# Performance work log

Hardware: AMD Instinct MI355X
Metric: run time of the kernel (lower is better)

Reference implementation:

```python
import jax, jax.numpy as jnp
import numpy as np

B, T = 32, 50
H, D, V = 1024, 512, 50257


def setup_inputs() -> dict:
    key = jax.random.key(0)
    ks = jax.random.split(key, 8)
    s = 0.05  # small init scale to keep LSTM gates in a sane range
    return {
        "inputs": jax.random.normal(ks[0], (B, H), jnp.float32),          # initial hidden state
        "targets": jax.random.randint(ks[1], (B, T), 0, V, jnp.int32),     # teacher-forcing tokens
        "emb": jax.random.normal(ks[2], (V, D), jnp.float32) * s,
        "W_ih": jax.random.normal(ks[3], (4 * H, D), jnp.float32) * s,     # torch gate order i,f,g,o
        "W_hh": jax.random.normal(ks[4], (4 * H, H), jnp.float32) * s,
        "b_ih": jnp.zeros((4 * H,), jnp.float32),
        "b_hh": jnp.zeros((4 * H,), jnp.float32),
        "W_proj": jax.random.normal(ks[5], (V, H), jnp.float32) * s,
        "b_proj": jnp.zeros((V,), jnp.float32),
    }


def reference(inputs, targets, emb, W_ih, W_hh, b_ih, b_hh, W_proj, b_proj):
    b, t = targets.shape
    h = inputs.shape[1]
    # decoder input tokens: BOS(=1) at step 0, then targets shifted right by one
    tok = jnp.concatenate([jnp.ones((b, 1), targets.dtype), targets[:, :-1]], axis=1)  # [B,T]
    x = emb[tok]  # [B,T,D]
    # precompute input contribution to all gates for every step
    xg = jnp.einsum("btd,gd->btg", x, W_ih) + b_ih + b_hh  # [B,T,4H]

    def step(carry, xg_t):
        hs, cs = carry
        g = xg_t + hs @ W_hh.T  # [B,4H]
        i = jax.nn.sigmoid(g[:, :h])
        f = jax.nn.sigmoid(g[:, h:2 * h])
        gg = jnp.tanh(g[:, 2 * h:3 * h])
        o = jax.nn.sigmoid(g[:, 3 * h:])
        cs = f * cs + i * gg
        hs = o * jnp.tanh(cs)
        return (hs, cs), hs

    c0 = jnp.zeros_like(inputs)
    _, hs = jax.lax.scan(step, (inputs, c0), jnp.swapaxes(xg, 0, 1))  # hs: [T,B,H]
    hs = jnp.swapaxes(hs, 0, 1)  # [B,T,H]
    logits = jnp.einsum("bth,vh->btv", hs, W_proj) + b_proj  # [B,T,V]
    predictions = jnp.argmax(logits, axis=-1)  # [B,T]
    return logits, predictions
```

## Files before the change

kernel.cpp:

```cpp
#include <hip/hip_runtime.h>
#include <math.h>

#define BB 32
#define TT 50
#define HH 1024
#define DD 512
#define VV 50257
#define G4H 4096

typedef __attribute__((ext_vector_type(8))) short bf16x8;
typedef __attribute__((ext_vector_type(8))) unsigned short u16x8;
typedef __attribute__((ext_vector_type(4))) float f32x4;

__device__ inline unsigned short f2bf(float x) {
    unsigned u = __float_as_uint(x);
    u = (u + 0x7fff + ((u >> 16) & 1)) >> 16;
    return (unsigned short)u;
}
__device__ inline float bf2f(unsigned short h) {
    return __uint_as_float(((unsigned)h) << 16);
}
__device__ inline void gl16(const void* g, void* l) {
    __builtin_amdgcn_global_load_lds(
        (const __attribute__((address_space(1))) unsigned int*)g,
        (__attribute__((address_space(3))) unsigned int*)l, 16, 0, 0);
}

__global__ void split_f32(const float* __restrict__ x,
                          unsigned short* __restrict__ hi,
                          unsigned short* __restrict__ lo, long n4) {
    long i = (long)blockIdx.x * 256 + threadIdx.x;
    long stride = (long)gridDim.x * 256;
    for (; i < n4; i += stride) {
        float4 v = ((const float4*)x)[i];
        ushort4 h, l;
        h.x = f2bf(v.x); l.x = f2bf(v.x - bf2f(h.x));
        h.y = f2bf(v.y); l.y = f2bf(v.y - bf2f(h.y));
        h.z = f2bf(v.z); l.z = f2bf(v.z - bf2f(h.z));
        h.w = f2bf(v.w); l.w = f2bf(v.w - bf2f(h.w));
        ((ushort4*)hi)[i] = h;
        ((ushort4*)lo)[i] = l;
    }
}

__global__ void xg_gemm(const int* __restrict__ targets,
                        const float* __restrict__ emb,
                        const float* __restrict__ W_ih,
                        const float* __restrict__ b_ih,
                        const float* __restrict__ b_hh,
                        float* __restrict__ xg) {
    __shared__ float As[16][65];
    __shared__ float Bs[16][65];
    const int m0 = blockIdx.y * 64;
    const int n0 = blockIdx.x * 64;
    const int tid = threadIdx.x;
    const int tx = tid & 15;
    const int ty = tid >> 4;
    const int lk = tx;
    const int lm = ty;

    const float* arow[4];
    const float* brow[4];
#pragma unroll
    for (int i = 0; i < 4; i++) {
        int bt = m0 + lm + i * 16;
        int b = bt / TT, t = bt % TT;
        int tok = (t == 0) ? 1 : targets[b * TT + (t - 1)];
        arow[i] = emb + (size_t)tok * DD;
        int n = n0 + lm + i * 16;
        brow[i] = W_ih + (size_t)n * DD;
    }

    float acc[4][4] = {};
    for (int k0 = 0; k0 < DD; k0 += 16) {
#pragma unroll
        for (int i = 0; i < 4; i++) As[lk][lm + i * 16] = arow[i][k0 + lk];
#pragma unroll
        for (int i = 0; i < 4; i++) Bs[lk][lm + i * 16] = brow[i][k0 + lk];
        __syncthreads();
#pragma unroll
        for (int k = 0; k < 16; k++) {
            float a[4], bb[4];
#pragma unroll
            for (int i = 0; i < 4; i++) a[i] = As[k][ty + i * 16];
#pragma unroll
            for (int j = 0; j < 4; j++) bb[j] = Bs[k][tx + j * 16];
#pragma unroll
            for (int i = 0; i < 4; i++)
#pragma unroll
                for (int j = 0; j < 4; j++) acc[i][j] += a[i] * bb[j];
        }
        __syncthreads();
    }
#pragma unroll
    for (int i = 0; i < 4; i++) {
        int m = m0 + ty + i * 16;
#pragma unroll
        for (int j = 0; j < 4; j++) {
            int n = n0 + tx + j * 16;
            xg[(size_t)m * G4H + n] = acc[i][j] + b_ih[n] + b_hh[n];
        }
    }
}

#define NH 16
__global__ __launch_bounds__(512, 2) void lstm_mfma(
    const unsigned short* __restrict__ Wh, const unsigned short* __restrict__ Wl,
    const float* __restrict__ xg,
    const unsigned short* __restrict__ hin_h, const unsigned short* __restrict__ hin_l,
    long hin_stride,
    float* __restrict__ c_buf,
    unsigned short* __restrict__ Ah, unsigned short* __restrict__ Al,
    int t) {
    __shared__ unsigned short sW[2][2][2][64 * 64];
    __shared__ unsigned short sH[2][2][2][32 * 64];
    __shared__ float gbuf[8][32][17];
    const int tid = threadIdx.x;
    const int w = tid >> 6;
    const int g = w & 3;
    const int h2 = w >> 2;
    const int l = tid & 63;
    const int lr = l & 15, lk = l >> 4;
    const int nh0 = blockIdx.x * NH;

    const int stid = tid & 255;
    const int sh2 = tid >> 8;
    const int kbase = sh2 * 512;

    const int wrow = stid >> 2;
    const int ws0 = (stid & 3) * 2;
    const int wg = wrow >> 4, wj = wrow & 15;
    const unsigned short* gWh = Wh + (size_t)(wg * HH + nh0 + wj) * HH + kbase + ws0 * 8;
    const unsigned short* gWl = Wl + (size_t)(wg * HH + nh0 + wj) * HH + kbase + ws0 * 8;
    const int wwb0 = wrow * 64 + ((ws0) ^ (wrow & 7)) * 8;
    const int wwb1 = wrow * 64 + ((ws0 + 1) ^ (wrow & 7)) * 8;

    const int hp = stid & 127;
    const int hrow = hp >> 2;
    const int hs0 = (hp & 3) * 2;
    const unsigned short* gH =
        ((stid < 128) ? hin_h : hin_l) + (size_t)hrow * hin_stride + kbase + hs0 * 8;
    const int hsel = (stid < 128) ? 0 : 1;
    const int hwb0 = hrow * 64 + ((hs0) ^ (hrow & 7)) * 8;
    const int hwb1 = hrow * 64 + ((hs0 + 1) ^ (hrow & 7)) * 8;

    f32x4 acc0 = (f32x4){0.f, 0.f, 0.f, 0.f};
    f32x4 acc1 = (f32x4){0.f, 0.f, 0.f, 0.f};

    u16x8 rWh0 = *(const u16x8*)gWh, rWh1 = *(const u16x8*)(gWh + 8);
    u16x8 rWl0 = *(const u16x8*)gWl, rWl1 = *(const u16x8*)(gWl + 8);
    u16x8 rH0  = *(const u16x8*)gH,  rH1  = *(const u16x8*)(gH + 8);
    *(u16x8*)&sW[sh2][0][0][wwb0] = rWh0; *(u16x8*)&sW[sh2][0][0][wwb1] = rWh1;
    *(u16x8*)&sW[sh2][0][1][wwb0] = rWl0; *(u16x8*)&sW[sh2][0][1][wwb1] = rWl1;
    if (hsel == 0) { *(u16x8*)&sH[sh2][0][0][hwb0] = rH0; *(u16x8*)&sH[sh2][0][0][hwb1] = rH1; }
    else           { *(u16x8*)&sH[sh2][0][1][hwb0] = rH0; *(u16x8*)&sH[sh2][0][1][hwb1] = rH1; }
    rWh0 = *(const u16x8*)(gWh + 64); rWh1 = *(const u16x8*)(gWh + 64 + 8);
    rWl0 = *(const u16x8*)(gWl + 64); rWl1 = *(const u16x8*)(gWl + 64 + 8);
    rH0  = *(const u16x8*)(gH + 64);  rH1  = *(const u16x8*)(gH + 64 + 8);

    int cur = 0;
#pragma unroll 1
    for (int it = 0; it < 8; it++) {
        __syncthreads();
        if (it < 7) {
            const int nxt = cur ^ 1;
            *(u16x8*)&sW[sh2][nxt][0][wwb0] = rWh0; *(u16x8*)&sW[sh2][nxt][0][wwb1] = rWh1;
            *(u16x8*)&sW[sh2][nxt][1][wwb0] = rWl0; *(u16x8*)&sW[sh2][nxt][1][wwb1] = rWl1;
            if (hsel == 0) { *(u16x8*)&sH[sh2][nxt][0][hwb0] = rH0; *(u16x8*)&sH[sh2][nxt][0][hwb1] = rH1; }
            else           { *(u16x8*)&sH[sh2][nxt][1][hwb0] = rH0; *(u16x8*)&sH[sh2][nxt][1][hwb1] = rH1; }
            const int kn = (it < 6) ? (it + 2) * 64 : 0;
            rWh0 = *(const u16x8*)(gWh + kn); rWh1 = *(const u16x8*)(gWh + kn + 8);
            rWl0 = *(const u16x8*)(gWl + kn); rWl1 = *(const u16x8*)(gWl + kn + 8);
            rH0  = *(const u16x8*)(gH + kn);  rH1  = *(const u16x8*)(gH + kn + 8);
        }
#pragma unroll
        for (int kk = 0; kk < 2; kk++) {
            const int rsl = ((kk * 4 + lk) ^ (lr & 7)) * 8;
            bf16x8 bh = *(const bf16x8*)&sW[h2][cur][0][(g * 16 + lr) * 64 + rsl];
            bf16x8 bl = *(const bf16x8*)&sW[h2][cur][1][(g * 16 + lr) * 64 + rsl];
            bf16x8 a0h = *(const bf16x8*)&sH[h2][cur][0][lr * 64 + rsl];
            bf16x8 a1h = *(const bf16x8*)&sH[h2][cur][0][(16 + lr) * 64 + rsl];
            bf16x8 a0l = *(const bf16x8*)&sH[h2][cur][1][lr * 64 + rsl];
            bf16x8 a1l = *(const bf16x8*)&sH[h2][cur][1][(16 + lr) * 64 + rsl];
            acc0 = __builtin_amdgcn_mfma_f32_16x16x32_bf16(a0h, bh, acc0, 0, 0, 0);
            acc0 = __builtin_amdgcn_mfma_f32_16x16x32_bf16(a0h, bl, acc0, 0, 0, 0);
            acc0 = __builtin_amdgcn_mfma_f32_16x16x32_bf16(a0l, bh, acc0, 0, 0, 0);
            acc1 = __builtin_amdgcn_mfma_f32_16x16x32_bf16(a1h, bh, acc1, 0, 0, 0);
            acc1 = __builtin_amdgcn_mfma_f32_16x16x32_bf16(a1h, bl, acc1, 0, 0, 0);
            acc1 = __builtin_amdgcn_mfma_f32_16x16x32_bf16(a1l, bh, acc1, 0, 0, 0);
        }
        cur ^= 1;
    }

    __syncthreads();
#pragma unroll
    for (int r = 0; r < 4; r++) {
        gbuf[w][lk * 4 + r][lr] = acc0[r];
        gbuf[w][16 + lk * 4 + r][lr] = acc1[r];
    }
    __syncthreads();

    {
        int b = tid >> 4, j = tid & 15;
        size_t xb = ((size_t)b * TT + t) * G4H + nh0 + j;
        float gi_ = gbuf[0][b][j] + gbuf[4][b][j] + xg[xb];
        float gf_ = gbuf[1][b][j] + gbuf[5][b][j] + xg[xb + HH];
        float gg_ = gbuf[2][b][j] + gbuf[6][b][j] + xg[xb + 2 * HH];
        float go_ = gbuf[3][b][j] + gbuf[7][b][j] + xg[xb + 3 * HH];

        float i_ = 1.f / (1.f + expf(-gi_));
        float f_ = 1.f / (1.f + expf(-gf_));
        float g_ = tanhf(gg_);
        float o_ = 1.f / (1.f + expf(-go_));

        int ci = b * HH + nh0 + j;
        float c_old = (t == 0) ? 0.f : c_buf[ci];
        float c_new = f_ * c_old + i_ * g_;
        float h_new = o_ * tanhf(c_new);
        c_buf[ci] = c_new;

        size_t ho = ((size_t)b * TT + t) * HH + nh0 + j;
        unsigned short hh = f2bf(h_new);
        Ah[ho] = hh;
        Al[ho] = f2bf(h_new - bf2f(hh));
    }
}

__global__ void lstm_step(const float* __restrict__ W_hh,
                          const float* __restrict__ xg,
                          const float* __restrict__ h_prev,
                          float* __restrict__ c_buf,
                          float* __restrict__ h_out,
                          float* __restrict__ hs_all,
                          int t) {
    __shared__ float h_s[32][68];
    __shared__ float w_s[32][68];
    const int tid = threadIdx.x;
    const int b = tid & 31;
    const int jl = tid >> 5;
    const int n0 = blockIdx.x * 8;
    const int n = n0 + jl;

    float acc[4] = {0.f, 0.f, 0.f, 0.f};
    for (int k0 = 0; k0 < HH; k0 += 64) {
#pragma unroll
        for (int i = 0; i < 2; i++) {
            int e = tid + i * 256;
            int r = e >> 4;
            int c = e & 15;
            float4 hv = *(const float4*)&h_prev[r * HH + k0 + c * 4];
            *(float4*)&h_s[r][c * 4] = hv;
            int gi = r >> 3, jj = r & 7;
            float4 wv = *(const float4*)&W_hh[(size_t)(gi * HH + n0 + jj) * HH + k0 + c * 4];
            *(float4*)&w_s[r][c * 4] = wv;
        }
        __syncthreads();
#pragma unroll
        for (int k = 0; k < 64; k += 4) {
            float4 hv = *(const float4*)&h_s[b][k];
            float4 w0 = *(const float4*)&w_s[jl][k];
            float4 w1 = *(const float4*)&w_s[8 + jl][k];
            float4 w2 = *(const float4*)&w_s[16 + jl][k];
            float4 w3 = *(const float4*)&w_s[24 + jl][k];
            acc[0] += hv.x * w0.x + hv.y * w0.y + hv.z * w0.z + hv.w * w0.w;
            acc[1] += hv.x * w1.x + hv.y * w1.y + hv.z * w1.z + hv.w * w1.w;
            acc[2] += hv.x * w2.x + hv.y * w2.y + hv.z * w2.z + hv.w * w2.w;
            acc[3] += hv.x * w3.x + hv.y * w3.y + hv.z * w3.z + hv.w * w3.w;
        }
        __syncthreads();
    }

    const int bt = b * TT + t;
    float gi_ = acc[0] + xg[(size_t)bt * G4H + n];
    float gf_ = acc[1] + xg[(size_t)bt * G4H + HH + n];
    float gg_ = acc[2] + xg[(size_t)bt * G4H + 2 * HH + n];
    float go_ = acc[3] + xg[(size_t)bt * G4H + 3 * HH + n];

    float i_ = 1.f / (1.f + expf(-gi_));
    float f_ = 1.f / (1.f + expf(-gf_));
    float g_ = tanhf(gg_);
    float o_ = 1.f / (1.f + expf(-go_));

    float c_old = (t == 0) ? 0.f : c_buf[b * HH + n];
    float c_new = f_ * c_old + i_ * g_;
    float h_new = o_ * tanhf(c_new);

    c_buf[b * HH + n] = c_new;
    h_out[b * HH + n] = h_new;
    hs_all[(size_t)bt * HH + n] = h_new;
}

__global__ __launch_bounds__(256, 4) void proj_mfma(
    const unsigned short* __restrict__ Ah, const unsigned short* __restrict__ Al,
    const unsigned short* __restrict__ Bh, const unsigned short* __restrict__ Bl,
    const float* __restrict__ b_proj, float* __restrict__ logits) {
    __shared__ __attribute__((aligned(16))) unsigned short sA[2][128 * 32];
    __shared__ __attribute__((aligned(16))) unsigned short sB[2][128 * 32];
    const int tid = threadIdx.x;
    const int w = tid >> 6;
    const int l = tid & 63;
    const int wr = w >> 1, wc = w & 1;
    const int lr = l & 15, lk = l >> 4;

    const int d = blockIdx.x;
    const int xcd = d & 7;
    const int k = d >> 3;
    const int ncnt = (xcd == 0) ? 50 : 49;
    const int nstart = (xcd == 0) ? 0 : 50 + (xcd - 1) * 49;
    if (k >= 13 * ncnt) return;
    const int per4 = 4 * ncnt;
    int s, rr_;
    if (k < per4)          { s = 0; rr_ = k; }
    else if (k < 2 * per4) { s = 1; rr_ = k - per4; }
    else if (k < 3 * per4) { s = 2; rr_ = k - 2 * per4; }
    else                   { s = 3; rr_ = k - 3 * per4; }
    const int ssize = (s == 3) ? 1 : 4;
    const int nloc = rr_ / ssize;
    const int mins = rr_ - nloc * ssize;
    const int m0 = (s * 4 + mins) * 128;
    const int n0 = (nstart + nloc) * 128;

    const unsigned short* garr = (w == 0) ? Ah : (w == 1) ? Al : (w == 2) ? Bh : Bl;
    unsigned short* larr = (w == 0) ? sA[0] : (w == 1) ? sA[1]
                         : (w == 2) ? sB[0] : sB[1];
    const int isA = (w < 2);
    const unsigned short* gsrc[8];
#pragma unroll
    for (int i = 0; i < 8; i++) {
        int r = i * 16 + (l >> 2);
        int sl = (l & 3) ^ ((r >> 1) & 3);
        int g = isA ? (m0 + r) : (n0 + r);
        int gmax = isA ? (BB * TT - 1) : (VV - 1);
        if (g > gmax) g = gmax;
        gsrc[i] = garr + (size_t)g * HH + sl * 8;
    }

    const int rswz = (lk ^ ((lr >> 1) & 3)) * 8;

    f32x4 acc[4][4];
#pragma unroll
    for (int i = 0; i < 4; i++)
#pragma unroll
        for (int j = 0; j < 4; j++) acc[i][j] = (f32x4){0.f, 0.f, 0.f, 0.f};

#pragma unroll 1
    for (int it = 0; it < 32; it++) {
        const int k0v = it * 32;
#pragma unroll
        for (int i = 0; i < 8; i++)
            gl16(gsrc[i] + k0v, larr + i * 512);
        __syncthreads();

        bf16x8 ah[4], al[4], bh[4], bl[4];
#pragma unroll
        for (int i = 0; i < 4; i++) {
            int ra = (wr * 64 + i * 16 + lr) * 32 + rswz;
            ah[i] = *(const bf16x8*)&sA[0][ra];
            al[i] = *(const bf16x8*)&sA[1][ra];
        }
#pragma unroll
        for (int j = 0; j < 4; j++) {
            int rb = (wc * 64 + j * 16 + lr) * 32 + rswz;
            bh[j] = *(const bf16x8*)&sB[0][rb];
            bl[j] = *(const bf16x8*)&sB[1][rb];
        }
#pragma unroll
        for (int i = 0; i < 4; i++)
#pragma unroll
            for (int j = 0; j < 4; j++) {
                acc[i][j] = __builtin_amdgcn_mfma_f32_16x16x32_bf16(ah[i], bh[j], acc[i][j], 0, 0, 0);
                acc[i][j] = __builtin_amdgcn_mfma_f32_16x16x32_bf16(ah[i], bl[j], acc[i][j], 0, 0, 0);
                acc[i][j] = __builtin_amdgcn_mfma_f32_16x16x32_bf16(al[i], bh[j], acc[i][j], 0, 0, 0);
            }
        __syncthreads();
    }

    float* ewave = ((float*)sA) + w * 1024;
    const int nn = n0 + wc * 64 + l;
    const float bpv = b_proj[nn < VV ? nn : VV - 1];
    const bool nok = (nn < VV);
#pragma unroll
    for (int i = 0; i < 4; i++) {
#pragma unroll
        for (int j = 0; j < 4; j++)
#pragma unroll
            for (int r2 = 0; r2 < 4; r2++)
                ewave[(lk * 4 + r2) * 64 + j * 16 + lr] = acc[i][j][r2];
#pragma unroll
        for (int rr = 0; rr < 16; rr++) {
            int m = m0 + wr * 64 + i * 16 + rr;
            float v = ewave[rr * 64 + l] + bpv;
            if (m < BB * TT && nok)
                logits[(size_t)m * VV + nn] = v;
        }
    }
}

__global__ void proj_gemm(const float* __restrict__ hs,
                          const float* __restrict__ W_proj,
                          const float* __restrict__ b_proj,
                          float* __restrict__ logits) {
    __shared__ float As[16][65];
    __shared__ float Bs[16][65];
    const int m0 = blockIdx.y * 64;
    const int n0 = blockIdx.x * 64;
    const int tid = threadIdx.x;
    const int tx = tid & 15;
    const int ty = tid >> 4;
    const int lk = tx;
    const int lm = ty;

    const float* arow[4];
    const float* brow[4];
    bool bval[4];
#pragma unroll
    for (int i = 0; i < 4; i++) {
        arow[i] = hs + (size_t)(m0 + lm + i * 16) * HH;
        int n = n0 + lm + i * 16;
        bval[i] = (n < VV);
        brow[i] = W_proj + (size_t)(bval[i] ? n : 0) * HH;
    }

    float acc[4][4] = {};
    for (int k0 = 0; k0 < HH; k0 += 16) {
#pragma unroll
        for (int i = 0; i < 4; i++) As[lk][lm + i * 16] = arow[i][k0 + lk];
#pragma unroll
        for (int i = 0; i < 4; i++)
            Bs[lk][lm + i * 16] = bval[i] ? brow[i][k0 + lk] : 0.f;
        __syncthreads();
#pragma unroll
        for (int k = 0; k < 16; k++) {
            float a[4], bb[4];
#pragma unroll
            for (int i = 0; i < 4; i++) a[i] = As[k][ty + i * 16];
#pragma unroll
            for (int j = 0; j < 4; j++) bb[j] = Bs[k][tx + j * 16];
#pragma unroll
            for (int i = 0; i < 4; i++)
#pragma unroll
                for (int j = 0; j < 4; j++) acc[i][j] += a[i] * bb[j];
        }
        __syncthreads();
    }
#pragma unroll
    for (int i = 0; i < 4; i++) {
        int m = m0 + ty + i * 16;
#pragma unroll
        for (int j = 0; j < 4; j++) {
            int n = n0 + tx + j * 16;
            if (n < VV)
                logits[(size_t)m * VV + n] = acc[i][j] + b_proj[n];
        }
    }
}

__global__ void argmax_kernel(const float* __restrict__ logits,
                              float* __restrict__ preds) {
    const int bt = blockIdx.x;
    const float* row = logits + (size_t)bt * VV;
    const int tid = threadIdx.x;

    float best = -INFINITY;
    int bidx = 0x7fffffff;
    for (int v = tid; v < VV; v += 256) {
        float x = row[v];
        if (x > best) { best = x; bidx = v; }
    }
    __shared__ float sv[256];
    __shared__ int si[256];
    sv[tid] = best;
    si[tid] = bidx;
    __syncthreads();
    for (int s = 128; s > 0; s >>= 1) {
        if (tid < s) {
            float ov = sv[tid + s];
            int oi = si[tid + s];
            if (ov > sv[tid] || (ov == sv[tid] && oi < si[tid])) {
                sv[tid] = ov;
                si[tid] = oi;
            }
        }
        __syncthreads();
    }
    if (tid == 0) preds[bt] = (float)si[0];
}

extern "C" void kernel_launch(void* const* d_in, const int* in_sizes, int n_in,
                              void* d_out, int out_size, void* d_ws, size_t ws_size,
                              hipStream_t stream) {
    const float* inputs = (const float*)d_in[0];
    const int*   targets = (const int*)d_in[1];
    const float* emb    = (const float*)d_in[2];
    const float* W_ih   = (const float*)d_in[3];
    const float* W_hh   = (const float*)d_in[4];
    const float* b_ih   = (const float*)d_in[5];
    const float* b_hh   = (const float*)d_in[6];
    const float* W_proj = (const float*)d_in[7];
    const float* b_proj = (const float*)d_in[8];

    float* out = (float*)d_out;
    float* logits = out;
    float* preds = out + (size_t)BB * TT * VV;

    float* ws = (float*)d_ws;
    float* xg = ws;
    float* cb = xg + (size_t)BB * TT * G4H;
    unsigned short* Ah = (unsigned short*)(cb + (size_t)BB * HH);
    unsigned short* Al = Ah + (size_t)BB * TT * HH;
    unsigned short* Bh = Al + (size_t)BB * TT * HH;
    unsigned short* Bl = Bh + (size_t)VV * HH;
    char* R = (char*)(Bl + (size_t)VV * HH);

    float* hs = (float*)R;
    float* h0 = hs + (size_t)BB * TT * HH;
    float* h1 = h0 + (size_t)BB * HH;
    unsigned short* Wh = (unsigned short*)R;
    unsigned short* Wl = Wh + (size_t)G4H * HH;
    unsigned short* iah = Wl + (size_t)G4H * HH;
    unsigned short* ial = iah + (size_t)BB * HH;

    size_t base = (char*)R - (char*)d_ws;
    size_t need1 = base + ((size_t)BB * TT * HH + 2 * (size_t)BB * HH) * 4;
    size_t need2 = base + (2 * (size_t)G4H * HH + 2 * (size_t)BB * HH) * 2;
    int mode = (ws_size >= need2) ? 2 : (ws_size >= need1) ? 1 : 0;

    if (mode >= 1) {
        split_f32<<<4096, 256, 0, stream>>>(W_proj, Bh, Bl, (long)VV * HH / 4);
    }
    if (mode == 2) {
        split_f32<<<2048, 256, 0, stream>>>(W_hh, Wh, Wl, (long)G4H * HH / 4);
        split_f32<<<32, 256, 0, stream>>>(inputs, iah, ial, (long)BB * HH / 4);
    }

    xg_gemm<<<dim3(64, 25), 256, 0, stream>>>(targets, emb, W_ih, b_ih, b_hh, xg);

    if (mode == 2) {
        for (int t = 0; t < TT; t++) {
            const unsigned short* hh = (t == 0) ? iah : (Ah + (size_t)(t - 1) * HH);
            const unsigned short* hl = (t == 0) ? ial : (Al + (size_t)(t - 1) * HH);
            long hstride = (t == 0) ? HH : (long)TT * HH;
            lstm_mfma<<<64, 512, 0, stream>>>(Wh, Wl, xg, hh, hl, hstride,
                                              cb, Ah, Al, t);
        }
        proj_mfma<<<5200, 256, 0, stream>>>(Ah, Al, Bh, Bl, b_proj, logits);
    } else {
        for (int t = 0; t < TT; t++) {
            const float* hp = (t == 0) ? inputs : ((t & 1) ? h0 : h1);
            float* ho = (t & 1) ? h1 : h0;
            lstm_step<<<128, 256, 0, stream>>>(W_hh, xg, hp, cb, ho, hs, t);
        }
        if (mode == 1) {
            split_f32<<<1600, 256, 0, stream>>>(hs, Ah, Al, (long)BB * TT * HH / 4);
            proj_mfma<<<5200, 256, 0, stream>>>(Ah, Al, Bh, Bl, b_proj, logits);
        } else {
            proj_gemm<<<dim3(786, 25), 256, 0, stream>>>(hs, W_proj, b_proj, logits);
        }
    }

    argmax_kernel<<<1600, 256, 0, stream>>>(logits, preds);
}
```

Baseline: 1.279 ms.

## Fuse per-timestep LSTM launches into one persistent kernel with grid flag barriers

Replaces the 50 per-step lstm_mfma launches with a single persistent kernel of 64 blocks that loops over timesteps. Steps are synchronised through per-block release/acquire flags in global memory. The cell state now stays in a register instead of being read and written in global memory each step. This removes the per-step launch overhead, but depends on all 64 blocks being resident at once and adds a spin-wait global barrier every step.

Result: slower. 1.763 ms (+37.9%).

```diff
diff --git a/kernel.cpp b/kernel.cpp
--- a/kernel.cpp
+++ b/kernel.cpp
@@ -104,14 +104,12 @@
 }
 
 #define NH 16
-__global__ __launch_bounds__(512, 2) void lstm_mfma(
+__global__ __launch_bounds__(512, 1) void lstm_persist(
     const unsigned short* __restrict__ Wh, const unsigned short* __restrict__ Wl,
     const float* __restrict__ xg,
-    const unsigned short* __restrict__ hin_h, const unsigned short* __restrict__ hin_l,
-    long hin_stride,
-    float* __restrict__ c_buf,
+    const unsigned short* __restrict__ iah, const unsigned short* __restrict__ ial,
     unsigned short* __restrict__ Ah, unsigned short* __restrict__ Al,
-    int t) {
+    int* __restrict__ flags) {
     __shared__ unsigned short sW[2][2][2][64 * 64];
     __shared__ unsigned short sH[2][2][2][32 * 64];
     __shared__ float gbuf[8][32][17];
@@ -138,91 +136,110 @@
     const int hp = stid & 127;
     const int hrow = hp >> 2;
     const int hs0 = (hp & 3) * 2;
-    const unsigned short* gH =
-        ((stid < 128) ? hin_h : hin_l) + (size_t)hrow * hin_stride + kbase + hs0 * 8;
     const int hsel = (stid < 128) ? 0 : 1;
     const int hwb0 = hrow * 64 + ((hs0) ^ (hrow & 7)) * 8;
     const int hwb1 = hrow * 64 + ((hs0 + 1) ^ (hrow & 7)) * 8;
 
-    f32x4 acc0 = (f32x4){0.f, 0.f, 0.f, 0.f};
-    f32x4 acc1 = (f32x4){0.f, 0.f, 0.f, 0.f};
-
-    u16x8 rWh0 = *(const u16x8*)gWh, rWh1 = *(const u16x8*)(gWh + 8);
-    u16x8 rWl0 = *(const u16x8*)gWl, rWl1 = *(const u16x8*)(gWl + 8);
-    u16x8 rH0  = *(const u16x8*)gH,  rH1  = *(const u16x8*)(gH + 8);
-    *(u16x8*)&sW[sh2][0][0][wwb0] = rWh0; *(u16x8*)&sW[sh2][0][0][wwb1] = rWh1;
-    *(u16x8*)&sW[sh2][0][1][wwb0] = rWl0; *(u16x8*)&sW[sh2][0][1][wwb1] = rWl1;
-    if (hsel == 0) { *(u16x8*)&sH[sh2][0][0][hwb0] = rH0; *(u16x8*)&sH[sh2][0][0][hwb1] = rH1; }
-    else           { *(u16x8*)&sH[sh2][0][1][hwb0] = rH0; *(u16x8*)&sH[sh2][0][1][hwb1] = rH1; }
-    rWh0 = *(const u16x8*)(gWh + 64); rWh1 = *(const u16x8*)(gWh + 64 + 8);
-    rWl0 = *(const u16x8*)(gWl + 64); rWl1 = *(const u16x8*)(gWl + 64 + 8);
-    rH0  = *(const u16x8*)(gH + 64);  rH1  = *(const u16x8*)(gH + 64 + 8);
-
-    int cur = 0;
+    const int eb = tid >> 4, ej = tid & 15;
+    float creg = 0.f;
+
+    for (int t = 0; t < TT; t++) {
+        const unsigned short* hb =
+            t ? (hsel ? Al + (size_t)(t - 1) * HH : Ah + (size_t)(t - 1) * HH)
+              : (hsel ? ial : iah);
+        const long hstride = t ? (long)TT * HH : (long)HH;
+        const unsigned short* gH = hb + (size_t)hrow * hstride + kbase + hs0 * 8;
+
+        f32x4 acc0 = (f32x4){0.f, 0.f, 0.f, 0.f};
+        f32x4 acc1 = (f32x4){0.f, 0.f, 0.f, 0.f};
+
+        u16x8 rWh0 = *(const u16x8*)gWh, rWh1 = *(const u16x8*)(gWh + 8);
+        u16x8 rWl0 = *(const u16x8*)gWl, rWl1 = *(const u16x8*)(gWl + 8);
+        u16x8 rH0  = *(const u16x8*)gH,  rH1  = *(const u16x8*)(gH + 8);
+        *(u16x8*)&sW[sh2][0][0][wwb0] = rWh0; *(u16x8*)&sW[sh2][0][0][wwb1] = rWh1;
+        *(u16x8*)&sW[sh2][0][1][wwb0] = rWl0; *(u16x8*)&sW[sh2][0][1][wwb1] = rWl1;
+        if (hsel == 0) { *(u16x8*)&sH[sh2][0][0][hwb0] = rH0; *(u16x8*)&sH[sh2][0][0][hwb1] = rH1; }
+        else           { *(u16x8*)&sH[sh2][0][1][hwb0] = rH0; *(u16x8*)&sH[sh2][0][1][hwb1] = rH1; }
+        rWh0 = *(const u16x8*)(gWh + 64); rWh1 = *(const u16x8*)(gWh + 64 + 8);
+        rWl0 = *(const u16x8*)(gWl + 64); rWl1 = *(const u16x8*)(gWl + 64 + 8);
+        rH0  = *(const u16x8*)(gH + 64);  rH1  = *(const u16x8*)(gH + 64 + 8);
+
+        int cur = 0;
 #pragma unroll 1
-    for (int it = 0; it < 8; it++) {
-        __syncthreads();
-        if (it < 7) {
-            const int nxt = cur ^ 1;
-            *(u16x8*)&sW[sh2][nxt][0][wwb0] = rWh0; *(u16x8*)&sW[sh2][nxt][0][wwb1] = rWh1;
-            *(u16x8*)&sW[sh2][nxt][1][wwb0] = rWl0; *(u16x8*)&sW[sh2][nxt][1][wwb1] = rWl1;
-            if (hsel == 0) { *(u16x8*)&sH[sh2][nxt][0][hwb0] = rH0; *(u16x8*)&sH[sh2][nxt][0][hwb1] = rH1; }
-            else           { *(u16x8*)&sH[sh2][nxt][1][hwb0] = rH0; *(u16x8*)&sH[sh2][nxt][1][hwb1] = rH1; }
-            const int kn = (it < 6) ? (it + 2) * 64 : 0;
-            rWh0 = *(const u16x8*)(gWh + kn); rWh1 = *(const u16x8*)(gWh + kn + 8);
-            rWl0 = *(const u16x8*)(gWl + kn); rWl1 = *(const u16x8*)(gWl + kn + 8);
-            rH0  = *(const u16x8*)(gH + kn);  rH1  = *(const u16x8*)(gH + kn + 8);
-        }
-#pragma unroll
-        for (int kk = 0; kk < 2; kk++) {
-            const int rsl = ((kk * 4 + lk) ^ (lr & 7)) * 8;
-            bf16x8 bh = *(const bf16x8*)&sW[h2][cur][0][(g * 16 + lr) * 64 + rsl];
-            bf16x8 bl = *(const bf16x8*)&sW[h2][cur][1][(g * 16 + lr) * 64 + rsl];
-            bf16x8 a0h = *(const bf16x8*)&sH[h2][cur][0][lr * 64 + rsl];
-            bf16x8 a1h = *(const bf16x8*)&sH[h2][cur][0][(16 + lr) * 64 + rsl];
-            bf16x8 a0l = *(const bf16x8*)&sH[h2][cur][1][lr * 64 + rsl];
-            bf16x8 a1l = *(const bf16x8*)&sH[h2][cur][1][(16 + lr) * 64 + rsl];
-            acc0 = __builtin_amdgcn_mfma_f32_16x16x32_bf16(a0h, bh, acc0, 0, 0, 0);
-            acc0 = __builtin_amdgcn_mfma_f32_16x16x32_bf16(a0h, bl, acc0, 0, 0, 0);
-            acc0 = __builtin_amdgcn_mfma_f32_16x16x32_bf16(a0l, bh, acc0, 0, 0, 0);
-            acc1 = __builtin_amdgcn_mfma_f32_16x16x32_bf16(a1h, bh, acc1, 0, 0, 0);
-            acc1 = __builtin_amdgcn_mfma_f32_16x16x32_bf16(a1h, bl, acc1, 0, 0, 0);
-            acc1 = __builtin_amdgcn_mfma_f32_16x16x32_bf16(a1l, bh, acc1, 0, 0, 0);
-        }
-        cur ^= 1;
-    }
-
-    __syncthreads();
-#pragma unroll
-    for (int r = 0; r < 4; r++) {
-        gbuf[w][lk * 4 + r][lr] = acc0[r];
-        gbuf[w][16 + lk * 4 + r][lr] = acc1[r];
-    }
-    __syncthreads();
-
-    {
-        int b = tid >> 4, j = tid & 15;
-        size_t xb = ((size_t)b * TT + t) * G4H + nh0 + j;
-        float gi_ = gbuf[0][b][j] + gbuf[4][b][j] + xg[xb];
-        float gf_ = gbuf[1][b][j] + gbuf[5][b][j] + xg[xb + HH];
-        float gg_ = gbuf[2][b][j] + gbuf[6][b][j] + xg[xb + 2 * HH];
-        float go_ = gbuf[3][b][j] + gbuf[7][b][j] + xg[xb + 3 * HH];
-
-        float i_ = 1.f / (1.f + expf(-gi_));
-        float f_ = 1.f / (1.f + expf(-gf_));
-        float g_ = tanhf(gg_);
-        float o_ = 1.f / (1.f + expf(-go_));
-
-        int ci = b * HH + nh0 + j;
-        float c_old = (t == 0) ? 0.f : c_buf[ci];
-        float c_new = f_ * c_old + i_ * g_;
-        float h_new = o_ * tanhf(c_new);
-        c_buf[ci] = c_new;
-
-        size_t ho = ((size_t)b * TT + t) * HH + nh0 + j;
-        unsigned short hh = f2bf(h_new);
-        Ah[ho] = hh;
-        Al[ho] = f2bf(h_new - bf2f(hh));
+        for (int it = 0; it < 8; it++) {
+            __syncthreads();
+            if (it < 7) {
+                const int nxt = cur ^ 1;
+                *(u16x8*)&sW[sh2][nxt][0][wwb0] = rWh0; *(u16x8*)&sW[sh2][nxt][0][wwb1] = rWh1;
+                *(u16x8*)&sW[sh2][nxt][1][wwb0] = rWl0; *(u16x8*)&sW[sh2][nxt][1][wwb1] = rWl1;
+                if (hsel == 0) { *(u16x8*)&sH[sh2][nxt][0][hwb0] = rH0; *(u16x8*)&sH[sh2][nxt][0][hwb1] = rH1; }
+                else           { *(u16x8*)&sH[sh2][nxt][1][hwb0] = rH0; *(u16x8*)&sH[sh2][nxt][1][hwb1] = rH1; }
+                const int kn = (it < 6) ? (it + 2) * 64 : 0;
+                rWh0 = *(const u16x8*)(gWh + kn); rWh1 = *(const u16x8*)(gWh + kn + 8);
+                rWl0 = *(const u16x8*)(gWl + kn); rWl1 = *(const u16x8*)(gWl + kn + 8);
+                rH0  = *(const u16x8*)(gH + kn);  rH1  = *(const u16x8*)(gH + kn + 8);
+            }
+#pragma unroll
+            for (int kk = 0; kk < 2; kk++) {
+                const int rsl = ((kk * 4 + lk) ^ (lr & 7)) * 8;
+                bf16x8 bh = *(const bf16x8*)&sW[h2][cur][0][(g * 16 + lr) * 64 + rsl];
+                bf16x8 bl = *(const bf16x8*)&sW[h2][cur][1][(g * 16 + lr) * 64 + rsl];
+                bf16x8 a0h = *(const bf16x8*)&sH[h2][cur][0][lr * 64 + rsl];
+                bf16x8 a1h = *(const bf16x8*)&sH[h2][cur][0][(16 + lr) * 64 + rsl];
+                bf16x8 a0l = *(const bf16x8*)&sH[h2][cur][1][lr * 64 + rsl];
+                bf16x8 a1l = *(const bf16x8*)&sH[h2][cur][1][(16 + lr) * 64 + rsl];
+                acc0 = __builtin_amdgcn_mfma_f32_16x16x32_bf16(a0h, bh, acc0, 0, 0, 0);
+                acc0 = __builtin_amdgcn_mfma_f32_16x16x32_bf16(a0h, bl, acc0, 0, 0, 0);
+                acc0 = __builtin_amdgcn_mfma_f32_16x16x32_bf16(a0l, bh, acc0, 0, 0, 0);
+                acc1 = __builtin_amdgcn_mfma_f32_16x16x32_bf16(a1h, bh, acc1, 0, 0, 0);
+                acc1 = __builtin_amdgcn_mfma_f32_16x16x32_bf16(a1h, bl, acc1, 0, 0, 0);
+                acc1 = __builtin_amdgcn_mfma_f32_16x16x32_bf16(a1l, bh, acc1, 0, 0, 0);
+            }
+            cur ^= 1;
+        }
+
+        __syncthreads();
+#pragma unroll
+        for (int r = 0; r < 4; r++) {
+            gbuf[w][lk * 4 + r][lr] = acc0[r];
+            gbuf[w][16 + lk * 4 + r][lr] = acc1[r];
+        }
+        __syncthreads();
+
+        {
+            size_t xb = ((size_t)eb * TT + t) * G4H + nh0 + ej;
+            float gi_ = gbuf[0][eb][ej] + gbuf[4][eb][ej] + xg[xb];
+            float gf_ = gbuf[1][eb][ej] + gbuf[5][eb][ej] + xg[xb + HH];
+            float gg_ = gbuf[2][eb][ej] + gbuf[6][eb][ej] + xg[xb + 2 * HH];
+            float go_ = gbuf[3][eb][ej] + gbuf[7][eb][ej] + xg[xb + 3 * HH];
+
+            float i_ = 1.f / (1.f + expf(-gi_));
+            float f_ = 1.f / (1.f + expf(-gf_));
+            float g_ = tanhf(gg_);
+            float o_ = 1.f / (1.f + expf(-go_));
+
+            float c_new = f_ * creg + i_ * g_;
+            float h_new = o_ * tanhf(c_new);
+            creg = c_new;
+
+            size_t ho = ((size_t)eb * TT + t) * HH + nh0 + ej;
+            unsigned short hh2 = f2bf(h_new);
+            Ah[ho] = hh2;
+            Al[ho] = f2bf(h_new - bf2f(hh2));
+        }
+
+        if (t < TT - 1) {
+            __threadfence();
+            __syncthreads();
+            if (tid == 0)
+                __hip_atomic_store(&flags[blockIdx.x * 32], t + 1,
+                                   __ATOMIC_RELEASE, __HIP_MEMORY_SCOPE_AGENT);
+            if (tid < 64) {
+                while (__hip_atomic_load(&flags[tid * 32], __ATOMIC_ACQUIRE,
+                                         __HIP_MEMORY_SCOPE_AGENT) < t + 1) {}
+            }
+            __syncthreads();
+        }
     }
 }
 
@@ -531,18 +548,13 @@
     if (mode == 2) {
         split_f32<<<2048, 256, 0, stream>>>(W_hh, Wh, Wl, (long)G4H * HH / 4);
         split_f32<<<32, 256, 0, stream>>>(inputs, iah, ial, (long)BB * HH / 4);
+        hipMemsetAsync((void*)cb, 0, 64 * 32 * sizeof(int), stream);
     }
 
     xg_gemm<<<dim3(64, 25), 256, 0, stream>>>(targets, emb, W_ih, b_ih, b_hh, xg);
 
     if (mode == 2) {
-        for (int t = 0; t < TT; t++) {
-            const unsigned short* hh = (t == 0) ? iah : (Ah + (size_t)(t - 1) * HH);
-            const unsigned short* hl = (t == 0) ? ial : (Al + (size_t)(t - 1) * HH);
-            long hstride = (t == 0) ? HH : (long)TT * HH;
-            lstm_mfma<<<64, 512, 0, stream>>>(Wh, Wl, xg, hh, hl, hstride,
-                                              cb, Ah, Al, t);
-        }
+        lstm_persist<<<64, 512, 0, stream>>>(Wh, Wl, xg, iah, ial, Ah, Al, (int*)cb);
         proj_mfma<<<5200, 256, 0, stream>>>(Ah, Al, Bh, Bl, b_proj, logits);
     } else {
         for (int t = 0; t < TT; t++) {
```

## Fuse argmax into projection GEMM epilogue via packed atomicMax keys

Applied to the files above, without the earlier changes.

The projection kernel epilogue now reduces each output row's 64-column slice with wave shuffles and publishes a packed (order-preserving float, inverted index) 64-bit key through atomicMax. A tiny finish kernel then unpacks the indices into predictions. This removes the separate argmax pass that re-read the full logits tensor, at the cost of extra shuffles, one atomic per row per wave, a memset, and a non-unrolled store loop in the epilogue.

After: 1.432 ms. 12.0% more time.

```diff
diff --git a/kernel.cpp b/kernel.cpp
--- a/kernel.cpp
+++ b/kernel.cpp
@@ -293,7 +293,8 @@
 __global__ __launch_bounds__(256, 4) void proj_mfma(
     const unsigned short* __restrict__ Ah, const unsigned short* __restrict__ Al,
     const unsigned short* __restrict__ Bh, const unsigned short* __restrict__ Bl,
-    const float* __restrict__ b_proj, float* __restrict__ logits) {
+    const float* __restrict__ b_proj, float* __restrict__ logits,
+    unsigned long long* __restrict__ keys) {
     __shared__ __attribute__((aligned(16))) unsigned short sA[2][128 * 32];
     __shared__ __attribute__((aligned(16))) unsigned short sB[2][128 * 32];
     const int tid = threadIdx.x;
@@ -386,14 +387,35 @@
 #pragma unroll
             for (int r2 = 0; r2 < 4; r2++)
                 ewave[(lk * 4 + r2) * 64 + j * 16 + lr] = acc[i][j][r2];
-#pragma unroll
+#pragma unroll 1
         for (int rr = 0; rr < 16; rr++) {
             int m = m0 + wr * 64 + i * 16 + rr;
             float v = ewave[rr * 64 + l] + bpv;
             if (m < BB * TT && nok)
                 logits[(size_t)m * VV + nn] = v;
-        }
-    }
+            float bv = nok ? v : -INFINITY;
+            int bn = nn;
+#pragma unroll
+            for (int off = 32; off >= 1; off >>= 1) {
+                float ov = __shfl_xor(bv, off);
+                int on = __shfl_xor(bn, off);
+                if (ov > bv || (ov == bv && on < bn)) { bv = ov; bn = on; }
+            }
+            if (l == 0 && m < BB * TT) {
+                unsigned u = __float_as_uint(bv);
+                unsigned sfl = (u & 0x80000000u) ? ~u : (u | 0x80000000u);
+                unsigned long long key =
+                    ((unsigned long long)sfl << 32) | (unsigned)(~bn);
+                atomicMax(&keys[m], key);
+            }
+        }
+    }
+}
+
+__global__ void argmax_finish(const unsigned long long* __restrict__ keys,
+                              float* __restrict__ preds, int n) {
+    int i = blockIdx.x * 256 + threadIdx.x;
+    if (i < n) preds[i] = (float)(~(unsigned)(keys[i] & 0xFFFFFFFFull));
 }
 
 __global__ void proj_gemm(const float* __restrict__ hs,
@@ -515,18 +537,24 @@
     float* hs = (float*)R;
     float* h0 = hs + (size_t)BB * TT * HH;
     float* h1 = h0 + (size_t)BB * HH;
+    unsigned long long* keys1 = (unsigned long long*)(h1 + (size_t)BB * HH);
     unsigned short* Wh = (unsigned short*)R;
     unsigned short* Wl = Wh + (size_t)G4H * HH;
     unsigned short* iah = Wl + (size_t)G4H * HH;
     unsigned short* ial = iah + (size_t)BB * HH;
+    unsigned long long* keys2 = (unsigned long long*)(ial + (size_t)BB * HH);
 
     size_t base = (char*)R - (char*)d_ws;
-    size_t need1 = base + ((size_t)BB * TT * HH + 2 * (size_t)BB * HH) * 4;
-    size_t need2 = base + (2 * (size_t)G4H * HH + 2 * (size_t)BB * HH) * 2;
+    size_t need1 = base + ((size_t)BB * TT * HH + 2 * (size_t)BB * HH) * 4
+                 + (size_t)BB * TT * 8;
+    size_t need2 = base + (2 * (size_t)G4H * HH + 2 * (size_t)BB * HH) * 2
+                 + (size_t)BB * TT * 8;
     int mode = (ws_size >= need2) ? 2 : (ws_size >= need1) ? 1 : 0;
+    unsigned long long* keys = (mode == 2) ? keys2 : keys1;
 
     if (mode >= 1) {
         split_f32<<<4096, 256, 0, stream>>>(W_proj, Bh, Bl, (long)VV * HH / 4);
+        hipMemsetAsync((void*)keys, 0, (size_t)BB * TT * 8, stream);
     }
     if (mode == 2) {
         split_f32<<<2048, 256, 0, stream>>>(W_hh, Wh, Wl, (long)G4H * HH / 4);
@@ -543,7 +571,8 @@
             lstm_mfma<<<64, 512, 0, stream>>>(Wh, Wl, xg, hh, hl, hstride,
                                               cb, Ah, Al, t);
         }
-        proj_mfma<<<5200, 256, 0, stream>>>(Ah, Al, Bh, Bl, b_proj, logits);
+        proj_mfma<<<5200, 256, 0, stream>>>(Ah, Al, Bh, Bl, b_proj, logits, keys);
+        argmax_finish<<<(BB * TT + 255) / 256, 256, 0, stream>>>(keys, preds, BB * TT);
     } else {
         for (int t = 0; t < TT; t++) {
             const float* hp = (t == 0) ? inputs : ((t & 1) ? h0 : h1);
@@ -552,11 +581,11 @@
         }
         if (mode == 1) {
             split_f32<<<1600, 256, 0, stream>>>(hs, Ah, Al, (long)BB * TT * HH / 4);
-            proj_mfma<<<5200, 256, 0, stream>>>(Ah, Al, Bh, Bl, b_proj, logits);
+            proj_mfma<<<5200, 256, 0, stream>>>(Ah, Al, Bh, Bl, b_proj, logits, keys);
+            argmax_finish<<<(BB * TT + 255) / 256, 256, 0, stream>>>(keys, preds, BB * TT);
         } else {
             proj_gemm<<<dim3(786, 25), 256, 0, stream>>>(hs, W_proj, b_proj, logits);
-        }
-    }
-
-    argmax_kernel<<<1600, 256, 0, stream>>>(logits, preds);
-}
+            argmax_kernel<<<1600, 256, 0, stream>>>(logits, preds);
+        }
+    }
+}
```
